# Optimization experiments

Hardware: AMD Instinct MI355X
Metric: run time of the kernel (lower is better)

Reference implementation:

```python
import jax, jax.numpy as jnp
import numpy as np

N_MODES = 512
LOOP_LENGTHS = [1]  # tbi.loop_lengths (single loop of delay 1)


def _bs_schedule(n_modes, loop_lengths):
    """Static application schedule, matching the torch loop order.

    Returns (theta index k, mode i, delay d) for each step, in the order the
    rotations are right-multiplied into the unitary: U = ((I @ R_{K-1}) @ ...) @ R_0.
    """
    K = sum(n_modes - d for d in loop_lengths)
    ks, iis, dds = [], [], []
    ci = K - 1
    for delay in reversed(loop_lengths):
        for i in reversed(range(n_modes - delay)):
            ks.append(ci)
            iis.append(i)
            dds.append(delay)
            ci -= 1
    return np.array(ks), np.array(iis), np.array(dds)


def setup_inputs() -> dict:
    key = jax.random.key(0)
    K = sum(N_MODES - d for d in LOOP_LENGTHS)  # 511 beam splitters
    thetas = jax.random.normal(key, (K,), dtype=jnp.float32)
    return {"thetas": thetas}


def reference(thetas):
    ks, iis, dds = _bs_schedule(N_MODES, LOOP_LENGTHS)
    # cos/sin gathered into application order
    c = jnp.cos(thetas)[ks]
    s = jnp.sin(thetas)[ks]
    ia = jnp.asarray(iis, dtype=jnp.int32)           # first mode of each rotation
    ib = jnp.asarray(iis + dds, dtype=jnp.int32)     # second mode (i + delay)

    U0 = jnp.eye(N_MODES, dtype=thetas.dtype)

    def step(U, xs):
        ck, sk, a, b = xs
        # Right-multiply by Givens rotation R with R[a,a]=c, R[a,b]=s, R[b,a]=-s, R[b,b]=c
        col_a = U[:, a]
        col_b = U[:, b]
        U = U.at[:, a].set(ck * col_a - sk * col_b)
        U = U.at[:, b].set(sk * col_a + ck * col_b)
        return U, None

    U, _ = jax.lax.scan(step, U0, (c, s, ia, ib))
    return U
```

## Files before the change

### kernel.cpp

```cpp
#include <hip/hip_runtime.h>

#define NM  512
#define KTH 511

__global__ __launch_bounds__(64) void unitary_rows(const float* __restrict__ thetas,
                                                   float* __restrict__ U) {
    const int r    = blockIdx.x;
    const int lane = threadIdx.x;

    __shared__ float row[NM];

    #pragma unroll
    for (int k = 0; k < NM / 64; ++k) row[lane + 64 * k] = 0.0f;
    __syncthreads();

    const int   L  = r;
    const float cr = (r < KTH) ? cosf(thetas[r]) : 1.0f;

    float sv[8], cv[8];
    float p = 1.0f;
    #pragma unroll
    for (int mm = 0; mm < 8; ++mm) {
        const int m = lane * 8 + mm;
        if (m < L) {
            const int   i  = r - 1 - m;
            const float th = thetas[i];
            sv[mm] = sinf(th);
            cv[mm] = cosf(th);
            p *= -sv[mm];
        } else {
            sv[mm] = 0.0f;
            cv[mm] = 0.0f;
        }
    }

    float x = p;
    #pragma unroll
    for (int off = 1; off < 64; off <<= 1) {
        const float y = __shfl_up(x, off, 64);
        if (lane >= off) x *= y;
    }
    float pre = __shfl_up(x, 1, 64);
    if (lane == 0) pre = 1.0f;

    float Q = cr * pre;
    #pragma unroll
    for (int mm = 0; mm < 8; ++mm) {
        const int m = lane * 8 + mm;
        if (m < L) {
            const int i = r - 1 - m;
            row[i + 1] = cv[mm] * Q;
            Q          = -sv[mm] * Q;
            if (m == L - 1) row[0] = Q;
        }
    }
    if (r == 0 && lane == 0) row[0] = cr;
    if (r < KTH && lane == 0) row[r + 1] = sinf(thetas[r]);
    __syncthreads();

    float4*       dst = (float4*)(U + (size_t)r * NM);
    const float4* src = (const float4*)row;
    dst[lane]      = src[lane];
    dst[lane + 64] = src[lane + 64];
}

extern "C" void kernel_launch(void* const* d_in, const int* in_sizes, int n_in,
                              void* d_out, int out_size, void* d_ws, size_t ws_size,
                              hipStream_t stream) {
    const float* thetas = (const float*)d_in[0];
    float*       U      = (float*)d_out;
    unitary_rows<<<NM, 64, 0, stream>>>(thetas, U);
}
```

Measured before the change: 55.88 us.

## Compute unitary entries from log-space prefix products of sines in two kernels

Moves the sine/cosine evaluation into a single-block setup kernel that builds prefix sums of log|sin| and sign-parity counts in a workspace. A second fully parallel kernel then writes each matrix entry independently as a ratio of prefix products, using exp of the log difference. This removes the redundant per-row trig evaluation and serial products, but adds a second launch and a serialized block-wide scan. The log/exp formulation can lose precision when products become very small, and it breaks if any sine is exactly zero.

```diff
diff --git a/kernel.cpp b/kernel.cpp
--- a/kernel.cpp
+++ b/kernel.cpp
@@ -1,67 +1,74 @@
 #include <hip/hip_runtime.h>
+#include <math.h>
 
 #define NM  512
 #define KTH 511
 
-__global__ __launch_bounds__(64) void unitary_rows(const float* __restrict__ thetas,
-                                                   float* __restrict__ U) {
-    const int r    = blockIdx.x;
-    const int lane = threadIdx.x;
 
-    __shared__ float row[NM];
+
+__global__ __launch_bounds__(512) void setup_tables(const float* __restrict__ thetas,
+                                                    float* __restrict__ ws) {
+    const int i = threadIdx.x;
+    float*  c   = ws;
+    float*  s   = ws + NM;
+    float*  LP  = ws + 2 * NM;
+    int*    NEG = (int*)(ws + 3 * NM);
+
+    float sv = 0.0f, cv = 1.0f;
+    if (i < KTH) {
+        const float th = thetas[i];
+        sv = sinf(th);
+        cv = cosf(th);
+    }
+    c[i] = cv;
+    s[i] = sv;
+
+    float a   = (i < KTH) ? logf(fabsf(sv)) : 0.0f;
+    int   neg = (i < KTH) ? (sv > 0.0f ? 1 : 0) : 0;
+
+    __shared__ float la[NM];
+    __shared__ int   na[NM];
+    la[i] = a;
+    na[i] = neg;
+    __syncthreads();
 
     #pragma unroll
-    for (int k = 0; k < NM / 64; ++k) row[lane + 64 * k] = 0.0f;
-    __syncthreads();
-
-    const int   L  = r;
-    const float cr = (r < KTH) ? cosf(thetas[r]) : 1.0f;
-
-    float sv[8], cv[8];
-    float p = 1.0f;
-    #pragma unroll
-    for (int mm = 0; mm < 8; ++mm) {
-        const int m = lane * 8 + mm;
-        if (m < L) {
-            const int   i  = r - 1 - m;
-            const float th = thetas[i];
-            sv[mm] = sinf(th);
-            cv[mm] = cosf(th);
-            p *= -sv[mm];
-        } else {
-            sv[mm] = 0.0f;
-            cv[mm] = 0.0f;
-        }
+    for (int off = 1; off < NM; off <<= 1) {
+        float tf = (i >= off) ? la[i - off] : 0.0f;
+        int   ti = (i >= off) ? na[i - off] : 0;
+        __syncthreads();
+        la[i] += tf;
+        na[i] += ti;
+        __syncthreads();
     }
 
-    float x = p;
-    #pragma unroll
-    for (int off = 1; off < 64; off <<= 1) {
-        const float y = __shfl_up(x, off, 64);
-        if (lane >= off) x *= y;
+    LP[i]  = (i == 0) ? 0.0f : la[i - 1];
+    NEG[i] = (i == 0) ? 0    : na[i - 1];
+}
+
+__global__ __launch_bounds__(256) void fill_unitary(const float* __restrict__ ws,
+                                                    float* __restrict__ U) {
+    const float* c   = ws;
+    const float* s   = ws + NM;
+    const float* LP  = ws + 2 * NM;
+    const int*   NEG = (const int*)(ws + 3 * NM);
+
+    const int idx = blockIdx.x * 256 + threadIdx.x;
+    const int r   = idx >> 9;
+    const int j   = idx & (NM - 1);
+
+    float out;
+    if (j > r + 1) {
+        out = 0.0f;
+    } else if (j == r + 1) {
+        out = s[r];
+    } else {
+        const float cj  = (j == 0) ? 1.0f : c[j - 1];
+        const float mag = __expf(LP[r] - LP[j]) * cj * c[r];
+        const int   par = (NEG[r] - NEG[j]) & 1;
+        out = par ? -mag : mag;
     }
-    float pre = __shfl_up(x, 1, 64);
-    if (lane == 0) pre = 1.0f;
-
-    float Q = cr * pre;
-    #pragma unroll
-    for (int mm = 0; mm < 8; ++mm) {
-        const int m = lane * 8 + mm;
-        if (m < L) {
-            const int i = r - 1 - m;
-            row[i + 1] = cv[mm] * Q;
-            Q          = -sv[mm] * Q;
-            if (m == L - 1) row[0] = Q;
-        }
-    }
-    if (r == 0 && lane == 0) row[0] = cr;
-    if (r < KTH && lane == 0) row[r + 1] = sinf(thetas[r]);
-    __syncthreads();
-
-    float4*       dst = (float4*)(U + (size_t)r * NM);
-    const float4* src = (const float4*)row;
-    dst[lane]      = src[lane];
-    dst[lane + 64] = src[lane + 64];
+    U[idx] = out;
 }
 
 extern "C" void kernel_launch(void* const* d_in, const int* in_sizes, int n_in,
@@ -69,5 +76,8 @@
                               hipStream_t stream) {
     const float* thetas = (const float*)d_in[0];
     float*       U      = (float*)d_out;
-    unitary_rows<<<NM, 64, 0, stream>>>(thetas, U);
+    float*       ws     = (float*)d_ws;
+
+    setup_tables<<<1, NM, 0, stream>>>(thetas, ws);
+    fill_unitary<<<(NM * NM) / 256, 256, 0, stream>>>(ws, U);
 }
```

Result: no change. 55.93 us (+0.1%).
